# Optimization experiments

Hardware: AMD Instinct MI355X
Metric: run time of the kernel (lower is better)

Reference implementation:

```python
import jax, jax.numpy as jnp
import numpy as np


def setup_inputs() -> dict:
    key = jax.random.key(0)
    kx, kq, kk, kv = jax.random.split(key, 4)
    d_model, d_head = 1024, 64
    x = jax.random.normal(kx, (4, 4096, d_model), dtype=jnp.float32)
    scale = 1.0 / np.sqrt(d_model)
    Wq = jax.random.normal(kq, (d_model, d_head), dtype=jnp.float32) * scale
    Wk = jax.random.normal(kk, (d_model, d_head), dtype=jnp.float32) * scale
    Wv = jax.random.normal(kv, (d_model, d_head), dtype=jnp.float32) * scale
    return {"x": x, "Wq": Wq, "Wk": Wk, "Wv": Wv}


def reference(x, Wq, Wk, Wv):
    # x: [B, S, D]; Wq/Wk/Wv: [D, H]
    d_head = Wq.shape[-1]
    Q = jnp.einsum('bsd,dh->bsh', x, Wq)
    K = jnp.einsum('bsd,dh->bsh', x, Wk)
    V = jnp.einsum('bsd,dh->bsh', x, Wv)
    scores = jnp.einsum('bqh,bkh->bqk', Q, K) / jnp.sqrt(jnp.float32(d_head))
    S = x.shape[1]
    causal = jnp.tril(jnp.ones((S, S), dtype=bool))  # [S, S]
    scores = jnp.where(causal, scores, -jnp.inf)
    weights = jax.nn.softmax(scores, axis=-1)  # [B, S, S]
    return jnp.einsum('bqk,bkh->bqh', weights, V)
```

## Files before the change

### kernel.cpp

```cpp
#include <hip/hip_runtime.h>

#define D_MODEL 1024
#define D_HEAD  64
#define SEQ     4096
#define BATCH   4
#define M_TOT   (BATCH * SEQ)
#define LOG2E   1.44269504088896f
#define MFIX_L2 17.3123404906676f
#define CHUNK   16

typedef __bf16 bf16;
typedef bf16  bf16x8 __attribute__((ext_vector_type(8)));
typedef bf16  bf16x4v __attribute__((ext_vector_type(4)));
typedef float f32x4  __attribute__((ext_vector_type(4)));

#define MFMA(a, b, c) __builtin_amdgcn_mfma_f32_16x16x32_bf16(a, b, c, 0, 0, 0)

__device__ __forceinline__ void barrier_release_lds() {
    __builtin_amdgcn_sched_barrier(0);
    asm volatile("s_waitcnt lgkmcnt(0)" ::: "memory");
    __builtin_amdgcn_s_barrier();
    __builtin_amdgcn_sched_barrier(0);
}

#define QKV_OFF  0
#define OBUF_OFF 6291456
#define LBUF_OFF 10485760
#define WT_OFF   10551296
#define VT_OFF   10944512

__global__ void prep_kernel(const float* __restrict__ Wq, const float* __restrict__ Wk,
                            const float* __restrict__ Wv, bf16* __restrict__ Wt,
                            float4* __restrict__ zp, int n4)
{
    const int bx = blockIdx.x;
    const int t  = threadIdx.x;
    if (bx < 48) {
        __shared__ bf16 tr[64][72];
        const int wm = bx >> 4, kt = bx & 15, k0 = kt * 64;
        const float* W = (wm == 0) ? Wq : (wm == 1) ? Wk : Wv;
        const int kr = t >> 2, nb = (t & 3) * 16;
        #pragma unroll
        for (int j = 0; j < 4; j++) {
            float4 wrow = *(const float4*)(W + (size_t)(k0 + kr) * D_HEAD + nb + j * 4);
            tr[nb + j * 4 + 0][kr] = (bf16)wrow.x;
            tr[nb + j * 4 + 1][kr] = (bf16)wrow.y;
            tr[nb + j * 4 + 2][kr] = (bf16)wrow.z;
            tr[nb + j * 4 + 3][kr] = (bf16)wrow.w;
        }
        __syncthreads();
        const int n = t >> 2, kc = (t & 3) * 8;
        bf16* dst = Wt + (size_t)(wm * 64 + n) * D_MODEL + k0;
        #pragma unroll
        for (int h = 0; h < 2; h++) {
            bf16x8 v;
            #pragma unroll
            for (int j = 0; j < 8; j++) v[j] = tr[n][kc + h * 32 + j];
            *(bf16x8*)(dst + kc + h * 32) = v;
        }
    } else {
        int i = (bx - 48) * 256 + t;
        if (i < n4) zp[i] = float4{0.f, 0.f, 0.f, 0.f};
    }
}

#define PXP 40

__global__ __launch_bounds__(256) void proj_kernel(
    const float* __restrict__ x, const bf16* __restrict__ Wt,
    bf16* __restrict__ qkv, bf16* __restrict__ vt)
{
    __shared__ __align__(16) bf16 xs[2][32][PXP];
    __shared__ __align__(16) bf16 ws[2][192][PXP];

    const int t    = threadIdx.x;
    const int nw   = t >> 6;
    const int lane = t & 63;
    const int quad = lane >> 4;
    const int l15  = lane & 15;
    const int row0 = blockIdx.x * 32;

    const int xrow = t >> 3, xk4 = (t & 7) * 4;
    const float* xg = x + (size_t)(row0 + xrow) * D_MODEL + xk4;

    f32x4 acc[6] = {};

    float4 xaA, xaB;
    bf16x8 wtvA[3], wtvB[3];

    auto loadA = [&](int c) {
        xaA = *(const float4*)(xg + c * 32);
        #pragma unroll
        for (int it = 0; it < 3; it++) {
            int id = t + it * 256, n = id >> 2, k8 = (id & 3) * 8;
            wtvA[it] = *(const bf16x8*)(Wt + (size_t)n * D_MODEL + c * 32 + k8);
        }
    };
    auto loadB = [&](int c) {
        xaB = *(const float4*)(xg + c * 32);
        #pragma unroll
        for (int it = 0; it < 3; it++) {
            int id = t + it * 256, n = id >> 2, k8 = (id & 3) * 8;
            wtvB[it] = *(const bf16x8*)(Wt + (size_t)n * D_MODEL + c * 32 + k8);
        }
    };
    auto storeA = [&](int p) {
        bf16x4v xv;
        xv[0] = (bf16)xaA.x; xv[1] = (bf16)xaA.y;
        xv[2] = (bf16)xaA.z; xv[3] = (bf16)xaA.w;
        *(bf16x4v*)&xs[p][xrow][xk4] = xv;
        #pragma unroll
        for (int it = 0; it < 3; it++) {
            int id = t + it * 256, n = id >> 2, k8 = (id & 3) * 8;
            *(bf16x8*)&ws[p][n][k8] = wtvA[it];
        }
    };
    auto storeB = [&](int p) {
        bf16x4v xv;
        xv[0] = (bf16)xaB.x; xv[1] = (bf16)xaB.y;
        xv[2] = (bf16)xaB.z; xv[3] = (bf16)xaB.w;
        *(bf16x4v*)&xs[p][xrow][xk4] = xv;
        #pragma unroll
        for (int it = 0; it < 3; it++) {
            int id = t + it * 256, n = id >> 2, k8 = (id & 3) * 8;
            *(bf16x8*)&ws[p][n][k8] = wtvB[it];
        }
    };
    auto compute = [&](int p) {
        bf16x8 af[2], bfr[3];
        #pragma unroll
        for (int rg = 0; rg < 2; rg++)
            af[rg] = *(bf16x8*)&xs[p][rg * 16 + l15][quad * 8];
        #pragma unroll
        for (int j = 0; j < 3; j++)
            bfr[j] = *(bf16x8*)&ws[p][nw * 48 + j * 16 + l15][quad * 8];
        #pragma unroll
        for (int rg = 0; rg < 2; rg++)
            #pragma unroll
            for (int j = 0; j < 3; j++)
                acc[rg * 3 + j] = MFMA(af[rg], bfr[j], acc[rg * 3 + j]);
    };

    loadA(0);
    storeA(0);
    loadB(1);
    loadA(2);
    barrier_release_lds();

    int p = 0;
    for (int c = 0; c < 32; c += 2) {
        compute(p);
        storeB(p ^ 1);
        if (c + 3 < 32) loadB(c + 3);
        barrier_release_lds();
        p ^= 1;
        compute(p);
        if (c + 2 < 32) storeA(p ^ 1);
        if (c + 4 < 32) loadA(c + 4);
        barrier_release_lds();
        p ^= 1;
    }

    const int bb = row0 >> 12, s0 = row0 & (SEQ - 1);
    #pragma unroll
    for (int rg = 0; rg < 2; rg++)
        #pragma unroll
        for (int j = 0; j < 3; j++) {
            const int col = nw * 48 + j * 16 + l15;
            const int wm = col >> 6, h = col & 63;
            if (wm == 2) {
                bf16x4v vv;
                #pragma unroll
                for (int r = 0; r < 4; r++)
                    vv[r] = (bf16)acc[rg * 3 + j][r];
                *(bf16x4v*)(vt + ((size_t)bb * D_HEAD + h) * SEQ +
                            s0 + rg * 16 + quad * 4) = vv;
            } else {
                const float sc = (wm == 0) ? 0.125f : 1.0f;
                bf16* outp = qkv + (size_t)wm * M_TOT * D_HEAD;
                #pragma unroll
                for (int r = 0; r < 4; r++) {
                    const int row = row0 + rg * 16 + quad * 4 + r;
                    outp[(size_t)row * D_HEAD + h] =
                        (bf16)(acc[rg * 3 + j][r] * sc);
                }
            }
        }
}

__global__ __launch_bounds__(256, 4) void attn_kernel(
    const bf16* __restrict__ qkv, const bf16* __restrict__ vt,
    float* __restrict__ o_buf, float* __restrict__ l_buf)
{
    const int i = blockIdx.x;
    const int c = blockIdx.y;
    const int b = blockIdx.z;
    const int ntiles = i + 1;
    const int tile0  = c * CHUNK;
    if (tile0 >= ntiles) return;
    const int tile1 = min(tile0 + CHUNK, ntiles);

    __shared__ __align__(16) char KsB[2 * 64 * 128];
    __shared__ __align__(16) char VsB[2 * 64 * 128];

    auto kaddr = [](char* base, int pp, int row, int colb) -> void* {
        return base + pp * 8192 + row * 128 + (colb ^ ((row & 7) << 4));
    };

    const bf16* Q = qkv;
    const bf16* K = qkv + (size_t)M_TOT * D_HEAD;

    const int t    = threadIdx.x;
    const int wv   = t >> 6;
    const int lane = t & 63;
    const int quad = lane >> 4;
    const int l15  = lane & 15;
    const int qb   = i * 64;
    const size_t base  = (size_t)b * SEQ * D_HEAD;
    const bf16* vtb = vt + (size_t)b * D_HEAD * SEQ;

    bf16x8 qf0, qf1;
    {
        const bf16* qr = Q + base + (size_t)(qb + wv * 16 + l15) * D_HEAD;
        qf0 = *(const bf16x8*)(qr + quad * 8);
        qf1 = *(const bf16x8*)(qr + 32 + quad * 8);
    }

    f32x4 o[4] = {};
    float lsum = 0.f;
    const int qw0 = qb + wv * 16;

    const int dr  = t >> 2;
    const int cb  = (t & 3) * 16;

    bf16x8 kr0, kr1, vr0, vr1;
    auto load_kv = [&](int tile) {
        const bf16* kp = K + base + (size_t)(tile * 64 + dr) * D_HEAD;
        kr0 = *(const bf16x8*)(kp + (cb >> 1));
        kr1 = *(const bf16x8*)(kp + (cb >> 1) + 32);
        const bf16* vp = vtb + (size_t)dr * SEQ + tile * 64;
        vr0 = *(const bf16x8*)(vp + (cb >> 1));
        vr1 = *(const bf16x8*)(vp + (cb >> 1) + 32);
    };
    auto store_kv = [&](int pp) {
        *(bf16x8*)kaddr(KsB, pp, dr, cb)      = kr0;
        *(bf16x8*)kaddr(KsB, pp, dr, cb + 64) = kr1;
        *(bf16x8*)kaddr(VsB, pp, dr, cb)      = vr0;
        *(bf16x8*)kaddr(VsB, pp, dr, cb + 64) = vr1;
    };

    load_kv(tile0);
    store_kv(0);
    if (tile0 + 1 < tile1) load_kv(tile0 + 1);
    barrier_release_lds();

    int p = 0;
    for (int tile = tile0; tile < tile1; tile++) {
        const int kk0 = tile * 64;

        f32x4 sc4[4];
        __builtin_amdgcn_s_setprio(1);
        #pragma unroll
        for (int kt = 0; kt < 4; kt++) {
            f32x4 z = {};
            z = MFMA(*(bf16x8*)kaddr(KsB, p, kt * 16 + l15, quad * 16),      qf0, z);
            z = MFMA(*(bf16x8*)kaddr(KsB, p, kt * 16 + l15, 64 + quad * 16), qf1, z);
            sc4[kt] = z;
        }
        __builtin_amdgcn_s_setprio(0);

        bf16 ph[4][4];
        if (tile == i) {
            #pragma unroll
            for (int kt = 0; kt < 4; kt++)
                #pragma unroll
                for (int r = 0; r < 4; r++) {
                    float s = sc4[kt][r];
                    if (kk0 + kt * 16 + quad * 4 + r > qw0 + l15)
                        s = -1e30f;
                    float pe = __builtin_amdgcn_exp2f(fmaf(s, LOG2E, -MFIX_L2));
                    lsum += pe;
                    ph[kt][r] = (bf16)pe;
                }
        } else {
            #pragma unroll
            for (int kt = 0; kt < 4; kt++)
                #pragma unroll
                for (int r = 0; r < 4; r++) {
                    float pe = __builtin_amdgcn_exp2f(
                        fmaf(sc4[kt][r], LOG2E, -MFIX_L2));
                    lsum += pe;
                    ph[kt][r] = (bf16)pe;
                }
        }

        unsigned pku[4][2];
        #pragma unroll
        for (int kt = 0; kt < 4; kt++) {
            __builtin_memcpy(&pku[kt][0], &ph[kt][0], 4);
            __builtin_memcpy(&pku[kt][1], &ph[kt][2], 4);
        }

        const int srcA = l15 + ((lane & 16) ? 32 : 0);
        const int srcB = srcA + 16;
        const bool hi  = (lane & 32) != 0;

        #pragma unroll
        for (int c2 = 0; c2 < 2; c2++) {
            unsigned xA0 = __shfl((int)pku[2 * c2][0],     srcA);
            unsigned xA1 = __shfl((int)pku[2 * c2][1],     srcA);
            unsigned yA0 = __shfl((int)pku[2 * c2 + 1][0], srcA);
            unsigned yA1 = __shfl((int)pku[2 * c2 + 1][1], srcA);
            unsigned xB0 = __shfl((int)pku[2 * c2][0],     srcB);
            unsigned xB1 = __shfl((int)pku[2 * c2][1],     srcB);
            unsigned yB0 = __shfl((int)pku[2 * c2 + 1][0], srcB);
            unsigned yB1 = __shfl((int)pku[2 * c2 + 1][1], srcB);
            unsigned fr[4];
            fr[0] = hi ? yA0 : xA0;
            fr[1] = hi ? yA1 : xA1;
            fr[2] = hi ? yB0 : xB0;
            fr[3] = hi ? yB1 : xB1;
            bf16x8 pa;
            __builtin_memcpy(&pa, fr, 16);

            __builtin_amdgcn_s_setprio(1);
            #pragma unroll
            for (int t4 = 0; t4 < 4; t4++) {
                bf16x8 vb = *(bf16x8*)kaddr(VsB, p, t4 * 16 + l15,
                                            c2 * 64 + quad * 16);
                o[t4] = MFMA(pa, vb, o[t4]);
            }
            __builtin_amdgcn_s_setprio(0);
        }

        if (tile + 1 < tile1) {
            store_kv(p ^ 1);
            if (tile + 2 < tile1) load_kv(tile + 2);
            barrier_release_lds();
        }
        p ^= 1;
    }

    const int mrow0 = b * SEQ + qw0;
    lsum += __shfl_xor(lsum, 16, 64);
    lsum += __shfl_xor(lsum, 32, 64);
    if (lane < 16)
        atomicAdd(&l_buf[mrow0 + l15], lsum);
    #pragma unroll
    for (int r = 0; r < 4; r++) {
        const size_t orow = (size_t)(mrow0 + quad * 4 + r) * D_HEAD;
        #pragma unroll
        for (int t4 = 0; t4 < 4; t4++)
            atomicAdd(&o_buf[orow + t4 * 16 + l15], o[t4][r]);
    }
}

__global__ void norm_kernel(const float4* __restrict__ o_buf,
                            const float* __restrict__ l_buf,
                            float4* __restrict__ out)
{
    int gid = blockIdx.x * 256 + threadIdx.x;
    int m = gid >> 4;
    float inv = 1.0f / l_buf[m];
    float4 v = o_buf[gid];
    out[gid] = float4{v.x * inv, v.y * inv, v.z * inv, v.w * inv};
}

extern "C" void kernel_launch(void* const* d_in, const int* in_sizes, int n_in,
                              void* d_out, int out_size, void* d_ws, size_t ws_size,
                              hipStream_t stream) {
    const float* x  = (const float*)d_in[0];
    const float* Wq = (const float*)d_in[1];
    const float* Wk = (const float*)d_in[2];
    const float* Wv = (const float*)d_in[3];

    bf16*  qkv   = (bf16*)((char*)d_ws + QKV_OFF);
    float* o_buf = (float*)((char*)d_ws + OBUF_OFF);
    float* l_buf = (float*)((char*)d_ws + LBUF_OFF);
    bf16*  Wt    = (bf16*)((char*)d_ws + WT_OFF);
    bf16*  vt    = (bf16*)((char*)d_ws + VT_OFF);

    const int zero4 = (M_TOT * 65) / 4;
    const int zblocks = (zero4 + 255) / 256;
    prep_kernel<<<48 + zblocks, 256, 0, stream>>>(Wq, Wk, Wv, Wt,
                                                  (float4*)o_buf, zero4);
    proj_kernel<<<M_TOT / 32, 256, 0, stream>>>(x, Wt, qkv, vt);
    attn_kernel<<<dim3(SEQ / 64, SEQ / 64 / CHUNK, BATCH), 256, 0, stream>>>(
        qkv, vt, o_buf, l_buf);
    norm_kernel<<<M_TOT * 16 / 256, 256, 0, stream>>>((const float4*)o_buf, l_buf,
                                                      (float4*)d_out);
}
```

Before: 157.5 us.

## Load projection MFMA operands directly from global memory, dropping LDS staging

The QKV projection kernel no longer stages x and W tiles through shared memory with barriers. Each wave now loads its MFMA operand fragments straight from global memory into registers with a two-stage register double buffer. The grid is split into single-wave blocks over 4 column groups of 48. The aim is to remove LDS traffic and barrier stalls, at the cost of reading each x row four times from global/L2 and loading with narrower per-lane access patterns.

```diff
diff --git a/kernel.cpp b/kernel.cpp
--- a/kernel.cpp
+++ b/kernel.cpp
@@ -64,101 +64,77 @@
     }
 }
 
-#define PXP 40
-
-__global__ __launch_bounds__(256) void proj_kernel(
+__global__ __launch_bounds__(64, 4) void proj_kernel(
     const float* __restrict__ x, const bf16* __restrict__ Wt,
     bf16* __restrict__ qkv, bf16* __restrict__ vt)
 {
-    __shared__ __align__(16) bf16 xs[2][32][PXP];
-    __shared__ __align__(16) bf16 ws[2][192][PXP];
-
-    const int t    = threadIdx.x;
-    const int nw   = t >> 6;
-    const int lane = t & 63;
+    const int lane = threadIdx.x;
     const int quad = lane >> 4;
     const int l15  = lane & 15;
     const int row0 = blockIdx.x * 32;
-
-    const int xrow = t >> 3, xk4 = (t & 7) * 4;
-    const float* xg = x + (size_t)(row0 + xrow) * D_MODEL + xk4;
+    const int n0   = blockIdx.y * 48;
+
+    const float* xr0 = x + (size_t)(row0 + l15) * D_MODEL + quad * 8;
+    const float* xr1 = x + (size_t)(row0 + 16 + l15) * D_MODEL + quad * 8;
+    const bf16* wp0 = Wt + (size_t)(n0 + 0 * 16 + l15) * D_MODEL + quad * 8;
+    const bf16* wp1 = Wt + (size_t)(n0 + 1 * 16 + l15) * D_MODEL + quad * 8;
+    const bf16* wp2 = Wt + (size_t)(n0 + 2 * 16 + l15) * D_MODEL + quad * 8;
 
     f32x4 acc[6] = {};
 
-    float4 xaA, xaB;
-    bf16x8 wtvA[3], wtvB[3];
+    float4 a0A, a1A, b0A, b1A; bf16x8 w0A, w1A, w2A;
+    float4 a0B, a1B, b0B, b1B; bf16x8 w0B, w1B, w2B;
 
     auto loadA = [&](int c) {
-        xaA = *(const float4*)(xg + c * 32);
-        #pragma unroll
-        for (int it = 0; it < 3; it++) {
-            int id = t + it * 256, n = id >> 2, k8 = (id & 3) * 8;
-            wtvA[it] = *(const bf16x8*)(Wt + (size_t)n * D_MODEL + c * 32 + k8);
-        }
+        a0A = *(const float4*)(xr0 + c * 32);
+        a1A = *(const float4*)(xr0 + c * 32 + 4);
+        b0A = *(const float4*)(xr1 + c * 32);
+        b1A = *(const float4*)(xr1 + c * 32 + 4);
+        w0A = *(const bf16x8*)(wp0 + c * 32);
+        w1A = *(const bf16x8*)(wp1 + c * 32);
+        w2A = *(const bf16x8*)(wp2 + c * 32);
     };
     auto loadB = [&](int c) {
-        xaB = *(const float4*)(xg + c * 32);
-        #pragma unroll
-        for (int it = 0; it < 3; it++) {
-            int id = t + it * 256, n = id >> 2, k8 = (id & 3) * 8;
-            wtvB[it] = *(const bf16x8*)(Wt + (size_t)n * D_MODEL + c * 32 + k8);
-        }
-    };
-    auto storeA = [&](int p) {
-        bf16x4v xv;
-        xv[0] = (bf16)xaA.x; xv[1] = (bf16)xaA.y;
-        xv[2] = (bf16)xaA.z; xv[3] = (bf16)xaA.w;
-        *(bf16x4v*)&xs[p][xrow][xk4] = xv;
-        #pragma unroll
-        for (int it = 0; it < 3; it++) {
-            int id = t + it * 256, n = id >> 2, k8 = (id & 3) * 8;
-            *(bf16x8*)&ws[p][n][k8] = wtvA[it];
-        }
-    };
-    auto storeB = [&](int p) {
-        bf16x4v xv;
-        xv[0] = (bf16)xaB.x; xv[1] = (bf16)xaB.y;
-        xv[2] = (bf16)xaB.z; xv[3] = (bf16)xaB.w;
-        *(bf16x4v*)&xs[p][xrow][xk4] = xv;
-        #pragma unroll
-        for (int it = 0; it < 3; it++) {
-            int id = t + it * 256, n = id >> 2, k8 = (id & 3) * 8;
-            *(bf16x8*)&ws[p][n][k8] = wtvB[it];
-        }
-    };
-    auto compute = [&](int p) {
-        bf16x8 af[2], bfr[3];
-        #pragma unroll
-        for (int rg = 0; rg < 2; rg++)
-            af[rg] = *(bf16x8*)&xs[p][rg * 16 + l15][quad * 8];
-        #pragma unroll
-        for (int j = 0; j < 3; j++)
-            bfr[j] = *(bf16x8*)&ws[p][nw * 48 + j * 16 + l15][quad * 8];
-        #pragma unroll
-        for (int rg = 0; rg < 2; rg++)
-            #pragma unroll
-            for (int j = 0; j < 3; j++)
-                acc[rg * 3 + j] = MFMA(af[rg], bfr[j], acc[rg * 3 + j]);
+        a0B = *(const float4*)(xr0 + c * 32);
+        a1B = *(const float4*)(xr0 + c * 32 + 4);
+        b0B = *(const float4*)(xr1 + c * 32);
+        b1B = *(const float4*)(xr1 + c * 32 + 4);
+        w0B = *(const bf16x8*)(wp0 + c * 32);
+        w1B = *(const bf16x8*)(wp1 + c * 32);
+        w2B = *(const bf16x8*)(wp2 + c * 32);
+    };
+    auto cvt8 = [](float4 lo, float4 hi) {
+        bf16x8 r;
+        r[0] = (bf16)lo.x; r[1] = (bf16)lo.y; r[2] = (bf16)lo.z; r[3] = (bf16)lo.w;
+        r[4] = (bf16)hi.x; r[5] = (bf16)hi.y; r[6] = (bf16)hi.z; r[7] = (bf16)hi.w;
+        return r;
+    };
+    auto computeA = [&]() {
+        bf16x8 af0 = cvt8(a0A, a1A), af1 = cvt8(b0A, b1A);
+        acc[0] = MFMA(af0, w0A, acc[0]);
+        acc[1] = MFMA(af0, w1A, acc[1]);
+        acc[2] = MFMA(af0, w2A, acc[2]);
+        acc[3] = MFMA(af1, w0A, acc[3]);
+        acc[4] = MFMA(af1, w1A, acc[4]);
+        acc[5] = MFMA(af1, w2A, acc[5]);
+    };
+    auto computeB = [&]() {
+        bf16x8 af0 = cvt8(a0B, a1B), af1 = cvt8(b0B, b1B);
+        acc[0] = MFMA(af0, w0B, acc[0]);
+        acc[1] = MFMA(af0, w1B, acc[1]);
+        acc[2] = MFMA(af0, w2B, acc[2]);
+        acc[3] = MFMA(af1, w0B, acc[3]);
+        acc[4] = MFMA(af1, w1B, acc[4]);
+        acc[5] = MFMA(af1, w2B, acc[5]);
     };
 
     loadA(0);
-    storeA(0);
     loadB(1);
-    loadA(2);
-    barrier_release_lds();
-
-    int p = 0;
     for (int c = 0; c < 32; c += 2) {
-        compute(p);
-        storeB(p ^ 1);
+        computeA();
+        if (c + 2 < 32) loadA(c + 2);
+        computeB();
         if (c + 3 < 32) loadB(c + 3);
-        barrier_release_lds();
-        p ^= 1;
-        compute(p);
-        if (c + 2 < 32) storeA(p ^ 1);
-        if (c + 4 < 32) loadA(c + 4);
-        barrier_release_lds();
-        p ^= 1;
     }
 
     const int bb = row0 >> 12, s0 = row0 & (SEQ - 1);
@@ -166,7 +142,7 @@
     for (int rg = 0; rg < 2; rg++)
         #pragma unroll
         for (int j = 0; j < 3; j++) {
-            const int col = nw * 48 + j * 16 + l15;
+            const int col = n0 + j * 16 + l15;
             const int wm = col >> 6, h = col & 63;
             if (wm == 2) {
                 bf16x4v vv;
@@ -384,7 +360,7 @@
     const int zblocks = (zero4 + 255) / 256;
     prep_kernel<<<48 + zblocks, 256, 0, stream>>>(Wq, Wk, Wv, Wt,
                                                   (float4*)o_buf, zero4);
-    proj_kernel<<<M_TOT / 32, 256, 0, stream>>>(x, Wt, qkv, vt);
+    proj_kernel<<<dim3(M_TOT / 32, 4), 64, 0, stream>>>(x, Wt, qkv, vt);
     attn_kernel<<<dim3(SEQ / 64, SEQ / 64 / CHUNK, BATCH), 256, 0, stream>>>(
         qkv, vt, o_buf, l_buf);
     norm_kernel<<<M_TOT * 16 / 256, 256, 0, stream>>>((const float4*)o_buf, l_buf,
```

Result: slower. 177.6 us (+12.8%).
